# Kernel tuning notes

Hardware: AMD Instinct MI355X
Metric: run time of the kernel (lower is better)

The kernel has to match this reference:

```python
import jax, jax.numpy as jnp
import numpy as np
from jax.scipy.stats import norm

N_TOK, D_MODEL, N_EXP, N_SEL = 16384, 4096, 16, 4
NOISE_EPS = 0.01
LOSS_LAMBDA = 0.01


def setup_inputs() -> dict:
    key = jax.random.key(0)
    kx, k1, k2, kn, kz = jax.random.split(key, 5)
    x = jax.random.normal(kx, (N_TOK, D_MODEL), dtype=jnp.float32)
    w1 = jax.random.normal(k1, (N_EXP, D_MODEL), dtype=jnp.float32) * 0.02
    w2 = jax.random.normal(k2, (N_EXP, N_EXP), dtype=jnp.float32) * 0.02
    wn = jax.random.normal(kn, (N_EXP, D_MODEL), dtype=jnp.float32) * 0.02
    noise = jax.random.normal(kz, (N_TOK, N_EXP), dtype=jnp.float32)
    return {"x": x, "w1": w1, "w2": w2, "wn": wn, "noise": noise}


def _cv_squared(v, eps=1e-10):
    # torch .var() is unbiased (ddof=1)
    return jnp.var(v, ddof=1) / (jnp.mean(v) ** 2 + eps)


def reference(x, w1, w2, wn, noise):
    # MLP gate: Linear(D->E, no bias) -> tanh -> Linear(E->E, no bias)
    logits_gate = jnp.einsum("te,fe->tf", jnp.tanh(jnp.einsum("td,ed->te", x, w1)), w2)
    noise_control = jax.nn.softplus(jnp.einsum("td,ed->te", x, wn)) + NOISE_EPS
    logits_noise = noise * noise_control
    logits = logits_gate + logits_noise  # [T, E]

    m = min(N_SEL + 1, N_EXP)  # k+1 values for threshold computation
    top_logits, top_indices = jax.lax.top_k(logits, m)  # [T, m]
    top_k_logits = top_logits[:, :N_SEL]
    top_k_indices = top_indices[:, :N_SEL]
    top_k_scores = jax.nn.softmax(top_k_logits, axis=1)  # [T, k]

    # importance: scatter top-k scores back to dense [T, E]
    rows = jnp.arange(N_TOK)[:, None]
    scores_filtered = jnp.zeros_like(logits).at[rows, top_k_indices].set(top_k_scores)
    importance = scores_filtered.sum(0)  # [E]

    # load: smooth estimator via Normal CDF (faithful to source, which
    # compares logits_noise against the in/out thresholds)
    threshold_if_in = top_logits[:, N_SEL:N_SEL + 1]       # (k+1)-th top value, [T,1]
    threshold_if_out = top_logits[:, N_SEL - 1:N_SEL]      # k-th top value, [T,1]
    is_in = logits_noise > threshold_if_in
    prob_if_in = norm.cdf((logits_gate - threshold_if_in) / noise_control)
    prob_if_out = norm.cdf((logits_gate - threshold_if_out) / noise_control)
    prob = jnp.where(is_in, prob_if_in, prob_if_out)
    load = prob.sum(0)  # [E]

    gate_loss = LOSS_LAMBDA * (_cv_squared(importance) + _cv_squared(load))
    return top_k_indices, top_k_scores, gate_loss
```

## Files before the change

kernel.cpp:

```cpp
#include <hip/hip_runtime.h>
#include <math.h>

#define N_TOK   16384
#define D_MODEL 4096
#define N_EXP   16
#define N_SEL   4
#define WELEM   (N_EXP * D_MODEL)
#define TILES   2
#define NWIN    16
#define WINF    256
#define TSTR    260
#define BUFW    (32 * TSTR)

typedef __bf16 bf16x8 __attribute__((ext_vector_type(8)));
typedef float  f32x4  __attribute__((ext_vector_type(4)));

#define MFMA(a, b, c) __builtin_amdgcn_mfma_f32_16x16x32_bf16((a), (b), (c), 0, 0, 0)

__device__ __forceinline__ float4 ntload4(const float* p)
{
    const f32x4 v = __builtin_nontemporal_load((const f32x4*)p);
    return make_float4(v[0], v[1], v[2], v[3]);
}

__global__ __launch_bounds__(256) void wprep_kernel(const float* __restrict__ w1,
                                                    const float* __restrict__ wn,
                                                    __bf16* __restrict__ wbuf,
                                                    float* __restrict__ g_acc)
{
    const int i = blockIdx.x * 256 + threadIdx.x;
    if (blockIdx.x == 0 && threadIdx.x < 2 * N_EXP) g_acc[threadIdx.x] = 0.f;
    {
        const float v = w1[i];
        const __bf16 h = (__bf16)v;  const float r1 = v - (float)h;
        const __bf16 m = (__bf16)r1; const float r2 = r1 - (float)m;
        wbuf[i] = h; wbuf[WELEM + i] = m; wbuf[2 * WELEM + i] = (__bf16)r2;
    }
    {
        const float v = wn[i];
        const __bf16 h = (__bf16)v;  const float r1 = v - (float)h;
        const __bf16 m = (__bf16)r1; const float r2 = r1 - (float)m;
        wbuf[3 * WELEM + i] = h; wbuf[4 * WELEM + i] = m; wbuf[5 * WELEM + i] = (__bf16)r2;
    }
}

__device__ __forceinline__ void split8(const float4 a, const float4 b,
                                       bf16x8& h, bf16x8& m, bf16x8& l)
{
    const float v[8] = {a.x, a.y, a.z, a.w, b.x, b.y, b.z, b.w};
    #pragma unroll
    for (int j = 0; j < 8; ++j) {
        const float vv = v[j];
        const __bf16 hh = (__bf16)vv;  const float r1 = vv - (float)hh;
        const __bf16 mm = (__bf16)r1;  const float r2 = r1 - (float)mm;
        h[j] = hh; m[j] = mm; l[j] = (__bf16)r2;
    }
}

__global__ __launch_bounds__(512, 4) void gate_kernel(
    const float* __restrict__ x, const __bf16* __restrict__ wbuf,
    const float* __restrict__ w2, const float* __restrict__ noise,
    float* __restrict__ out, float* __restrict__ g_imp, float* __restrict__ g_load)
{
    __shared__ float smem[2 * BUFW];
    __shared__ float s_imp[N_EXP], s_ld[N_EXP];

    const int tid  = threadIdx.x;
    const int lane = tid & 63;
    const int wv   = tid >> 6;
    const int ml   = lane & 15;
    const int q    = lane >> 4;
    const int t0   = blockIdx.x * (TILES * 16);

    const __bf16* w1h = wbuf;
    const __bf16* w1m = wbuf + WELEM;
    const __bf16* w1l = wbuf + 2 * WELEM;
    const __bf16* wnh = wbuf + 3 * WELEM;
    const __bf16* wnm = wbuf + 4 * WELEM;
    const __bf16* wnl = wbuf + 5 * WELEM;

    const int wofc = ml * D_MODEL + wv * 32 + q * 8;

    int gi0, gi1, gi2, gi3, li0, li1, li2, li3;
    {
#define MAP(P, GI, LI)                                        \
        {   const int fid = (P) * 512 + tid;                  \
            const int tk  = fid >> 6;                         \
            const int sl  = fid & 63;                         \
            GI = (t0 + tk) * D_MODEL + sl * 4;                \
            LI = tk * TSTR + sl * 4;  }
        MAP(0, gi0, li0) MAP(1, gi1, li1) MAP(2, gi2, li2) MAP(3, gi3, li3)
#undef MAP
    }
    const int lr0 = ml * TSTR + wv * 32 + q * 8;
    const int lr1 = (16 + ml) * TSTR + wv * 32 + q * 8;

    f32x4 c1[TILES], c2[TILES];
    #pragma unroll
    for (int tt = 0; tt < TILES; ++tt) {
        c1[tt] = (f32x4){0.f, 0.f, 0.f, 0.f};
        c2[tt] = (f32x4){0.f, 0.f, 0.f, 0.f};
    }

    float* bufA = smem;
    float* bufB = smem + BUFW;

    {
        const float4 s0 = ntload4(x + gi0);
        const float4 s1 = ntload4(x + gi1);
        const float4 s2 = ntload4(x + gi2);
        const float4 s3 = ntload4(x + gi3);
        *(float4*)(bufA + li0) = s0;
        *(float4*)(bufA + li1) = s1;
        *(float4*)(bufA + li2) = s2;
        *(float4*)(bufA + li3) = s3;
        __syncthreads();
    }

#define STEP(CUR, NXT, C)                                                     \
    {                                                                          \
        float4 sg0, sg1, sg2, sg3;                                             \
        if ((C) < NWIN - 1) {                                                  \
            const int co = ((C) + 1) * WINF;                                   \
            sg0 = ntload4(x + gi0 + co);                                       \
            sg1 = ntload4(x + gi1 + co);                                       \
            sg2 = ntload4(x + gi2 + co);                                       \
            sg3 = ntload4(x + gi3 + co);                                       \
        }                                                                      \
        const int wo = wofc + (C) * WINF;                                      \
        const bf16x8 a1h = *(const bf16x8*)(w1h + wo);                         \
        const bf16x8 a1m = *(const bf16x8*)(w1m + wo);                         \
        const bf16x8 a1l = *(const bf16x8*)(w1l + wo);                         \
        const bf16x8 a2h = *(const bf16x8*)(wnh + wo);                         \
        const bf16x8 a2m = *(const bf16x8*)(wnm + wo);                         \
        const bf16x8 a2l = *(const bf16x8*)(wnl + wo);                         \
        const float4 xa0 = *(const float4*)((CUR) + lr0);                      \
        const float4 xb0 = *(const float4*)((CUR) + lr0 + 4);                  \
        const float4 xa1 = *(const float4*)((CUR) + lr1);                      \
        const float4 xb1 = *(const float4*)((CUR) + lr1 + 4);                  \
        bf16x8 xh0, xm0, xl0, xh1, xm1, xl1;                                   \
        split8(xa0, xb0, xh0, xm0, xl0);                                       \
        split8(xa1, xb1, xh1, xm1, xl1);                                       \
        c1[0] = MFMA(a1h, xh0, c1[0]);  c2[0] = MFMA(a2h, xh0, c2[0]);         \
        c1[1] = MFMA(a1h, xh1, c1[1]);  c2[1] = MFMA(a2h, xh1, c2[1]);         \
        c1[0] = MFMA(a1h, xm0, c1[0]);  c2[0] = MFMA(a2h, xm0, c2[0]);         \
        c1[1] = MFMA(a1h, xm1, c1[1]);  c2[1] = MFMA(a2h, xm1, c2[1]);         \
        c1[0] = MFMA(a1m, xh0, c1[0]);  c2[0] = MFMA(a2m, xh0, c2[0]);         \
        c1[1] = MFMA(a1m, xh1, c1[1]);  c2[1] = MFMA(a2m, xh1, c2[1]);         \
        c1[0] = MFMA(a1h, xl0, c1[0]);  c2[0] = MFMA(a2h, xl0, c2[0]);         \
        c1[1] = MFMA(a1h, xl1, c1[1]);  c2[1] = MFMA(a2h, xl1, c2[1]);         \
        c1[0] = MFMA(a1l, xh0, c1[0]);  c2[0] = MFMA(a2l, xh0, c2[0]);         \
        c1[1] = MFMA(a1l, xh1, c1[1]);  c2[1] = MFMA(a2l, xh1, c2[1]);         \
        c1[0] = MFMA(a1m, xm0, c1[0]);  c2[0] = MFMA(a2m, xm0, c2[0]);         \
        c1[1] = MFMA(a1m, xm1, c1[1]);  c2[1] = MFMA(a2m, xm1, c2[1]);         \
        if ((C) < NWIN - 1) {                                                  \
            *(float4*)((NXT) + li0) = sg0;                                     \
            *(float4*)((NXT) + li1) = sg1;                                     \
            *(float4*)((NXT) + li2) = sg2;                                     \
            *(float4*)((NXT) + li3) = sg3;                                     \
        }                                                                      \
        __syncthreads();                                                       \
    }

    #pragma unroll
    for (int h = 0; h < NWIN / 2; ++h) {
        STEP(bufA, bufB, 2 * h)
        STEP(bufB, bufA, 2 * h + 1)
    }
#undef STEP

    float* red  = smem;
    float* dsum = smem + 8448;

    #pragma unroll
    for (int tt = 0; tt < TILES; ++tt) {
        #pragma unroll
        for (int r = 0; r < 4; ++r) {
            red[((wv * TILES + tt) * 16 + ml) * 33 + q * 4 + r]      = c1[tt][r];
            red[((wv * TILES + tt) * 16 + ml) * 33 + 16 + q * 4 + r] = c2[tt][r];
        }
    }
    __syncthreads();

    for (int idx = tid; idx < TILES * 512; idx += 512) {
        const int tt = idx >> 9, tk = (idx >> 5) & 15, o = idx & 31;
        float s = 0.f;
        #pragma unroll
        for (int w = 0; w < 8; ++w) s += red[((w * TILES + tt) * 16 + tk) * 33 + o];
        dsum[(tt * 16 + tk) * 33 + o] = s;
    }
    if (tid < N_EXP) { s_imp[tid] = 0.f; s_ld[tid] = 0.f; }
    __syncthreads();

    if (tid < TILES * 16) {
        const int tt = tid >> 4, tk = tid & 15;
        const int t = t0 + tid;
        float dot[32];
        #pragma unroll
        for (int e = 0; e < 32; ++e) dot[e] = dsum[(tt * 16 + tk) * 33 + e];

        float th[N_EXP], nc[N_EXP];
        #pragma unroll
        for (int e = 0; e < N_EXP; ++e) th[e] = tanhf(dot[e]);
        #pragma unroll
        for (int e = 0; e < N_EXP; ++e) {
            const float v = dot[N_EXP + e];
            nc[e] = fmaxf(v, 0.f) + log1pf(expf(-fabsf(v))) + 0.01f;
        }

        float lg[N_EXP];
        #pragma unroll
        for (int f = 0; f < N_EXP; ++f) {
            float s = 0.f;
            #pragma unroll
            for (int e = 0; e < N_EXP; ++e) s = fmaf(th[e], w2[f * 16 + e], s);
            lg[f] = s;
        }

        float ln[N_EXP], v[N_EXP];
        {
            const float4* nz = (const float4*)(noise + (size_t)t * 16);
            const float4 n0 = nz[0], n1 = nz[1], n2 = nz[2], n3 = nz[3];
            const float nzv[16] = {n0.x, n0.y, n0.z, n0.w, n1.x, n1.y, n1.z, n1.w,
                                   n2.x, n2.y, n2.z, n2.w, n3.x, n3.y, n3.z, n3.w};
            #pragma unroll
            for (int e = 0; e < N_EXP; ++e) {
                ln[e] = nzv[e] * nc[e];
                v[e]  = lg[e] + ln[e];
            }
        }

        float tv[5]; int ti[5];
        #pragma unroll
        for (int j = 0; j < 5; ++j) {
            float best = -INFINITY; int bi = 0;
            #pragma unroll
            for (int e = 0; e < N_EXP; ++e) {
                bool taken = false;
                #pragma unroll
                for (int jj = 0; jj < 5; ++jj)
                    if (jj < j) taken = taken || (ti[jj] == e);
                if (!taken && v[e] > best) { best = v[e]; bi = e; }
            }
            tv[j] = best; ti[j] = bi;
        }

        const float mx = tv[0];
        float ex[4], ssum = 0.f;
        #pragma unroll
        for (int j = 0; j < 4; ++j) { ex[j] = expf(tv[j] - mx); ssum += ex[j]; }
        const float inv = 1.f / ssum;
        float sc[4];
        #pragma unroll
        for (int j = 0; j < 4; ++j) sc[j] = ex[j] * inv;

        #pragma unroll
        for (int j = 0; j < 4; ++j) atomicAdd(&s_imp[ti[j]], sc[j]);

        const float thr_in = tv[4], thr_out = tv[3];
        #pragma unroll
        for (int e = 0; e < N_EXP; ++e) {
            const bool  is_in = ln[e] > thr_in;
            const float thr   = is_in ? thr_in : thr_out;
            const float z     = (lg[e] - thr) / nc[e];
            const float prob  = 0.5f * (1.f + erff(z * 0.70710678118654752f));
            atomicAdd(&s_ld[e], prob);
        }

        ((float4*)out)[t] = make_float4((float)ti[0], (float)ti[1],
                                        (float)ti[2], (float)ti[3]);
        ((float4*)(out + N_TOK * N_SEL))[t] = make_float4(sc[0], sc[1], sc[2], sc[3]);
    }
    __syncthreads();
    if (tid < N_EXP)            atomicAdd(&g_imp[tid], s_imp[tid]);
    else if (tid < 2 * N_EXP)   atomicAdd(&g_load[tid - N_EXP], s_ld[tid - N_EXP]);
}

__global__ void loss_kernel(const float* __restrict__ g_imp,
                            const float* __restrict__ g_load,
                            float* __restrict__ out)
{
    if (threadIdx.x == 0 && blockIdx.x == 0) {
        double mi = 0.0, ml = 0.0;
        for (int e = 0; e < N_EXP; ++e) { mi += g_imp[e]; ml += g_load[e]; }
        mi /= N_EXP; ml /= N_EXP;
        double vi = 0.0, vl = 0.0;
        for (int e = 0; e < N_EXP; ++e) {
            const double di = g_imp[e] - mi;  vi += di * di;
            const double dl = g_load[e] - ml; vl += dl * dl;
        }
        vi /= (N_EXP - 1); vl /= (N_EXP - 1);
        const double ci = vi / (mi * mi + 1e-10);
        const double cl = vl / (ml * ml + 1e-10);
        out[N_TOK * N_SEL * 2] = (float)(0.01 * (ci + cl));
    }
}

extern "C" void kernel_launch(void* const* d_in, const int* in_sizes, int n_in,
                              void* d_out, int out_size, void* d_ws, size_t ws_size,
                              hipStream_t stream)
{
    const float* x     = (const float*)d_in[0];
    const float* w1    = (const float*)d_in[1];
    const float* w2    = (const float*)d_in[2];
    const float* wn    = (const float*)d_in[3];
    const float* noise = (const float*)d_in[4];
    float* out = (float*)d_out;

    __bf16* wbuf  = (__bf16*)d_ws;
    float*  g_imp = (float*)((char*)d_ws + (1 << 20));
    float*  g_load = g_imp + N_EXP;

    wprep_kernel<<<WELEM / 256, 256, 0, stream>>>(w1, wn, wbuf, g_imp);
    gate_kernel<<<N_TOK / (TILES * 16), 512, 0, stream>>>(x, wbuf, w2, noise, out,
                                                          g_imp, g_load);
    loss_kernel<<<1, 64, 0, stream>>>(g_imp, g_load, out);
}
```

Before: 402.7 us.

## Deepen x prefetch to two windows ahead and use LDS-only barriers

The main loop now keeps two register sets of global x loads in flight, loading the window two steps ahead while the current window is consumed from LDS. The full __syncthreads is replaced by a barrier that waits only on LDS traffic (lgkmcnt) so outstanding global loads are not drained at each step. This aims to hide global-memory latency in the memory-bound gate GEMM, at the cost of extra registers, which may lower occupancy under the 512x4 launch bounds.

```diff
diff --git a/kernel.cpp b/kernel.cpp
--- a/kernel.cpp
+++ b/kernel.cpp
@@ -57,6 +57,10 @@
     }
 }
 
+#define SOFT_BARRIER()                                          \
+    asm volatile("s_waitcnt lgkmcnt(0)" ::: "memory");          \
+    __builtin_amdgcn_s_barrier();
+
 __global__ __launch_bounds__(512, 4) void gate_kernel(
     const float* __restrict__ x, const __bf16* __restrict__ wbuf,
     const float* __restrict__ w2, const float* __restrict__ noise,
@@ -105,35 +109,41 @@
     float* bufA = smem;
     float* bufB = smem + BUFW;
 
+    float4 pA0 = {}, pA1 = {}, pA2 = {}, pA3 = {};
+    float4 qA0 = {}, qA1 = {}, qA2 = {}, qA3 = {};
+
     {
-        const float4 s0 = ntload4(x + gi0);
-        const float4 s1 = ntload4(x + gi1);
-        const float4 s2 = ntload4(x + gi2);
-        const float4 s3 = ntload4(x + gi3);
-        *(float4*)(bufA + li0) = s0;
-        *(float4*)(bufA + li1) = s1;
-        *(float4*)(bufA + li2) = s2;
-        *(float4*)(bufA + li3) = s3;
-        __syncthreads();
-    }
-
-#define STEP(CUR, NXT, C)                                                     \
+        const float4 t0v = ntload4(x + gi0);
+        const float4 t1v = ntload4(x + gi1);
+        const float4 t2v = ntload4(x + gi2);
+        const float4 t3v = ntload4(x + gi3);
+        pA0 = ntload4(x + gi0 + WINF);
+        pA1 = ntload4(x + gi1 + WINF);
+        pA2 = ntload4(x + gi2 + WINF);
+        pA3 = ntload4(x + gi3 + WINF);
+        *(float4*)(bufA + li0) = t0v;
+        *(float4*)(bufA + li1) = t1v;
+        *(float4*)(bufA + li2) = t2v;
+        *(float4*)(bufA + li3) = t3v;
+        SOFT_BARRIER()
+    }
+
+#define STEP(CUR, NXT, C, P0, P1, P2, P3, Q0, Q1, Q2, Q3)                      \
     {                                                                          \
-        float4 sg0, sg1, sg2, sg3;                                             \
-        if ((C) < NWIN - 1) {                                                  \
-            const int co = ((C) + 1) * WINF;                                   \
-            sg0 = ntload4(x + gi0 + co);                                       \
-            sg1 = ntload4(x + gi1 + co);                                       \
-            sg2 = ntload4(x + gi2 + co);                                       \
-            sg3 = ntload4(x + gi3 + co);                                       \
-        }                                                                      \
-        const int wo = wofc + (C) * WINF;                                      \
+        const int wo = wofc + (C) * WINF;      \
         const bf16x8 a1h = *(const bf16x8*)(w1h + wo);                         \
         const bf16x8 a1m = *(const bf16x8*)(w1m + wo);                         \
         const bf16x8 a1l = *(const bf16x8*)(w1l + wo);                         \
         const bf16x8 a2h = *(const bf16x8*)(wnh + wo);                         \
         const bf16x8 a2m = *(const bf16x8*)(wnm + wo);                         \
         const bf16x8 a2l = *(const bf16x8*)(wnl + wo);                         \
+        if ((C) + 2 < NWIN) {                     \
+            const int co = ((C) + 2) * WINF;                                   \
+            Q0 = ntload4(x + gi0 + co);                                        \
+            Q1 = ntload4(x + gi1 + co);                                        \
+            Q2 = ntload4(x + gi2 + co);                                        \
+            Q3 = ntload4(x + gi3 + co);                                        \
+        }                                                                      \
         const float4 xa0 = *(const float4*)((CUR) + lr0);                      \
         const float4 xb0 = *(const float4*)((CUR) + lr0 + 4);                  \
         const float4 xa1 = *(const float4*)((CUR) + lr1);                      \
@@ -153,21 +163,22 @@
         c1[1] = MFMA(a1l, xh1, c1[1]);  c2[1] = MFMA(a2l, xh1, c2[1]);         \
         c1[0] = MFMA(a1m, xm0, c1[0]);  c2[0] = MFMA(a2m, xm0, c2[0]);         \
         c1[1] = MFMA(a1m, xm1, c1[1]);  c2[1] = MFMA(a2m, xm1, c2[1]);         \
-        if ((C) < NWIN - 1) {                                                  \
-            *(float4*)((NXT) + li0) = sg0;                                     \
-            *(float4*)((NXT) + li1) = sg1;                                     \
-            *(float4*)((NXT) + li2) = sg2;                                     \
-            *(float4*)((NXT) + li3) = sg3;                                     \
+        if ((C) + 1 < NWIN) {                   \
+            *(float4*)((NXT) + li0) = P0;      \
+            *(float4*)((NXT) + li1) = P1;      \
+            *(float4*)((NXT) + li2) = P2;      \
+            *(float4*)((NXT) + li3) = P3;                                      \
+            SOFT_BARRIER()                                                     \
         }                                                                      \
-        __syncthreads();                                                       \
     }
 
     #pragma unroll
     for (int h = 0; h < NWIN / 2; ++h) {
-        STEP(bufA, bufB, 2 * h)
-        STEP(bufB, bufA, 2 * h + 1)
+        STEP(bufA, bufB, 2 * h,     pA0, pA1, pA2, pA3, qA0, qA1, qA2, qA3)
+        STEP(bufB, bufA, 2 * h + 1, qA0, qA1, qA2, qA3, pA0, pA1, pA2, pA3)
     }
 #undef STEP
+    __syncthreads();
 
     float* red  = smem;
     float* dsum = smem + 8448;
```

After: 405.0 us. About the same (+0.6%).
